# Optimization experiments

Hardware: AMD Instinct MI355X
Metric: run time of the kernel (lower is better)

## Reference

```python
import jax, jax.numpy as jnp
import numpy as np

RADIUS = 9.0   # search_raduis_scale * particle_radius
K = 20         # N_neighbor
HIDDEN = [512, 512, 512, 512]


def embed(x, n_freqs):
    freqs = 2.0 ** jnp.arange(n_freqs, dtype=x.dtype)      # [F]
    xf = x[..., None, :] * freqs[:, None]                  # [..., F, C]
    sc = jnp.stack([jnp.sin(xf), jnp.cos(xf)], axis=-2)    # [..., F, 2, C]
    return jnp.concatenate([x, sc.reshape(*x.shape[:-1], -1)], axis=-1)


def ball_query(q, p, radius, k):
    # pytorch3d semantics: first k points (by index order) with squared dist < radius^2;
    # padding slots get dists=0, idx=-1, nn=0.
    n = p.shape[0]
    d2 = jnp.sum((q[:, None, :] - p[None, :, :]) ** 2, axis=-1)   # [P,N]
    valid = d2 < radius * radius
    score = jnp.where(valid, -jnp.arange(n, dtype=q.dtype), -jnp.inf)
    top, idx = jax.lax.top_k(score, k)                            # first k valid indices
    found = top > -jnp.inf
    safe = jnp.clip(idx, 0, n - 1)
    dists = jnp.where(found, jnp.take_along_axis(d2, safe, axis=1), 0.0)
    nn = jnp.where(found[..., None], p[safe], 0.0)                # [P,K,3]
    return dists, jnp.where(found, idx, -1), nn


def mlp(x, params):
    n = len(params)
    for l, (v, g, b) in enumerate(params):
        w = g * v / jnp.linalg.norm(v, axis=1, keepdims=True)     # weight_norm, dim=0
        x = x @ w.T + b
        if l < n - 1:
            x = jax.nn.relu(x)
    return jax.nn.sigmoid(x)


def setup_inputs() -> dict:
    key = jax.random.key(0)
    ks = jax.random.split(key, 32)
    R, S, N, F = 256, 128, 4096, 256
    P = R * S
    inp = {
        "points": jax.random.normal(ks[0], (P, 3), dtype=jnp.float32) * 3.0,
        "normals": jax.random.normal(ks[1], (P, 3), dtype=jnp.float32),
        "view_dirs": jax.random.normal(ks[2], (P, 3), dtype=jnp.float32),
        "feature_vectors": jax.random.normal(ks[3], (P, F), dtype=jnp.float32),
        "phys_points": jax.random.normal(ks[4], (N, 3), dtype=jnp.float32) * 3.0,
        "ray_dirs": jax.random.normal(ks[5], (R, 3), dtype=jnp.float32),
        "cam_loc": jax.random.normal(ks[6], (1, 3), dtype=jnp.float32),
    }
    d0 = 3 + 3 + 3 + F + 63 + 9 + 63 + 63 + 27 + 27   # = 517
    dims = [d0] + HIDDEN + [3]
    for l in range(len(dims) - 1):
        fan_in, fan_out = dims[l], dims[l + 1]
        inp[f"v{l}"] = jax.random.normal(ks[7 + l], (fan_out, fan_in), dtype=jnp.float32) * float(np.sqrt(2.0 / fan_out))
        inp[f"g{l}"] = jnp.ones((fan_out, 1), dtype=jnp.float32)
        inp[f"b{l}"] = jnp.zeros((fan_out,), dtype=jnp.float32)
    return inp


def reference(points, normals, view_dirs, feature_vectors, phys_points, ray_dirs, cam_loc,
              v0, g0, b0, v1, g1, b1, v2, g2, b2, v3, g3, b3, v4, g4, b4):
    params = [(v0, g0, b0), (v1, g1, b1), (v2, g2, b2), (v3, g3, b3), (v4, g4, b4)]
    # mode == 'idr'
    rendering_input = jnp.concatenate([points, view_dirs, normals, feature_vectors], axis=-1)
    dists, idx, neighbors = ball_query(points, phys_points, RADIUS, K)
    nn_mask = dists != 0                                             # [P,K]
    num_nn = nn_mask.sum(-1, keepdims=True).astype(points.dtype)     # [P,1]
    # smoothing_position (exclude_ray=True): Euclidean dists recomputed incl. zero-padded slots
    dd = jnp.linalg.norm(neighbors - points[:, None, :], axis=-1)    # [P,K]
    w = jnp.maximum(1.0 - (dd / RADIUS) ** 3, 0.0)
    smoothed_pos = (w[..., None] * neighbors).sum(-2) / (w.sum(-1, keepdims=True) + 1e-12)
    density = w.sum(-1, keepdims=True)                               # [P,1]
    d = smoothed_pos - cam_loc                                       # broadcast [P,3]
    smoothed_dir = d / jnp.linalg.norm(d, axis=-1, keepdims=True)
    # variance of masked neighbor offsets
    vec = jnp.where(nn_mask[..., None], neighbors - points[:, None, :], 0.0)
    vec_mean = vec.sum(-2) / (num_nn + 1e-12)                        # [P,3]
    var = jnp.where(nn_mask[..., None], (vec - vec_mean[:, None, :]) ** 2, 0.0).sum(-2) / (num_nn + 1e-12)
    reps = points.shape[0] // ray_dirs.shape[0]                      # samples per ray
    hit_dir_emb = jnp.repeat(embed(ray_dirs, 4), reps, axis=0)       # [P,27]
    feats = jnp.concatenate([embed(points, 10), embed(density, 4), embed(smoothed_pos, 10),
                             embed(var, 10), hit_dir_emb, embed(smoothed_dir, 4)], axis=-1)
    x = jnp.concatenate([rendering_input, feats], axis=-1)           # [P,517]
    return mlp(x, params)
```

## Files before the change

kernel.cpp:

```cpp
#include <hip/hip_runtime.h>
#include <hip/hip_bf16.h>

typedef unsigned short u16;
typedef short short8 __attribute__((ext_vector_type(8)));
typedef unsigned short ushort8 __attribute__((ext_vector_type(8)));
typedef float f32x4 __attribute__((ext_vector_type(4)));

static __device__ __forceinline__ u16 f2bf(float f) {
  unsigned u = __builtin_bit_cast(unsigned, f);
  unsigned r = (u + 0x7fffu + ((u >> 16) & 1u)) >> 16;
  return (u16)r;
}
static __device__ __forceinline__ float bf2f(u16 h) {
  unsigned u = ((unsigned)h) << 16;
  return __builtin_bit_cast(float, u);
}

static __device__ __forceinline__ void gload_lds16(const u16* g, u16* l) {
  __builtin_amdgcn_global_load_lds(
      (const __attribute__((address_space(1))) void*)g,
      (__attribute__((address_space(3))) void*)l, 16, 0, 0);
}


static __device__ void prep_w0_body(const float* __restrict__ v,
                                    const float* __restrict__ g,
                                    u16* __restrict__ out, int row, int lane) {
  double s = 0.0;
  for (int k = lane; k < 517; k += 64) {
    double x = (double)v[(size_t)row * 517 + k];
    s += x * x;
  }
#pragma unroll
  for (int off = 32; off; off >>= 1) s += __shfl_xor(s, off);
  double scale = (double)g[row] / sqrt(s);

  for (int j = lane; j < 576; j += 64) {
    int orig = -1;
    if (j < 256) {
      orig = 9 + j;
    } else if (j < 281) {
      int e = j - 256;
      if (e < 9)       orig = e;
      else if (e < 12) orig = 265 + (e - 9);
      else if (e == 12) orig = 328;
      else if (e < 16) orig = 337 + (e - 13);
      else if (e < 19) orig = 400 + (e - 16);
      else if (e < 22) orig = 463 + (e - 19);
      else if (e < 25) orig = 490 + (e - 22);
    } else if (j >= 288 && j < 524) {
      int t = j - 288;
      if (t < 60)       orig = 268 + t;
      else if (t < 68)  orig = 329 + (t - 60);
      else if (t < 128) orig = 340 + (t - 68);
      else if (t < 188) orig = 403 + (t - 128);
      else if (t < 212) orig = 466 + (t - 188);
      else if (t < 236) orig = 493 + (t - 212);
    }
    float wv = (orig >= 0) ? (float)((double)v[(size_t)row * 517 + orig] * scale) : 0.0f;
    out[(size_t)row * 576 + j] = f2bf(wv);
  }
}

static __device__ void prep_w_body(const float* __restrict__ v,
                                   const float* __restrict__ g,
                                   u16* __restrict__ out, int row, int lane) {
  double s = 0.0;
  for (int k = lane; k < 512; k += 64) {
    double x = (double)v[(size_t)row * 512 + k];
    s += x * x;
  }
#pragma unroll
  for (int off = 32; off; off >>= 1) s += __shfl_xor(s, off);
  double scale = (double)g[row] / sqrt(s);
  for (int k = lane; k < 512; k += 64)
    out[(size_t)row * 512 + k] = f2bf((float)((double)v[(size_t)row * 512 + k] * scale));
}

static __device__ void prep_w4_body(const float* __restrict__ v,
                                    const float* __restrict__ g,
                                    float* __restrict__ out, int row, int lane) {
  double s = 0.0;
  for (int k = lane; k < 512; k += 64) {
    double x = (double)v[(size_t)row * 512 + k];
    s += x * x;
  }
#pragma unroll
  for (int off = 32; off; off >>= 1) s += __shfl_xor(s, off);
  double scale = (double)g[row] / sqrt(s);
  for (int k = lane; k < 512; k += 64)
    out[(size_t)row * 512 + k] = (float)((double)v[(size_t)row * 512 + k] * scale);
}

static __device__ void build_tb_body(u16* __restrict__ TB, int lane) {
  for (int i = lane; i < 320; i += 64) {
    const int j = 256 + i;
    unsigned d = 0;
    if (j < 281) {
      int e = j - 256;
      int src = -1;
      if (e < 9)       src = e;
      else if (e < 12) src = e - 9;
      else if (e == 12) src = 9;
      else if (e < 16) src = 10 + (e - 13);
      else if (e < 19) src = 13 + (e - 16);
      else if (e < 22) src = 16 + (e - 19);
      else if (e < 25) src = 19 + (e - 22);
      if (src >= 0) d = 1u | ((unsigned)src << 2);
    } else if (j >= 288 && j < 524) {
      int t = j - 288;
      if (t < 236) {
        int base, src0;
        if (t < 60)       { base = 0;   src0 = 0;  }
        else if (t < 68)  { base = 60;  src0 = 9;  }
        else if (t < 128) { base = 68;  src0 = 10; }
        else if (t < 188) { base = 128; src0 = 13; }
        else if (t < 212) { base = 188; src0 = 16; }
        else              { base = 212; src0 = 19; }
        int u = t - base;
        int f, cs, src;
        if (src0 == 9) { f = u >> 1; cs = u & 1; src = 9; }
        else { f = u / 6; int r = u - 6 * f; cs = (r >= 3) ? 1 : 0; src = src0 + (cs ? r - 3 : r); }
        d = 2u | ((unsigned)src << 2) | ((unsigned)cs << 7) | ((unsigned)f << 8);
      }
    }
    TB[i] = (u16)d;
  }
}

__global__ void prep_all(const float* __restrict__ v0, const float* __restrict__ g0,
                         const float* __restrict__ v1, const float* __restrict__ g1,
                         const float* __restrict__ v2, const float* __restrict__ g2,
                         const float* __restrict__ v3, const float* __restrict__ g3,
                         const float* __restrict__ v4, const float* __restrict__ g4,
                         u16* __restrict__ W0, u16* __restrict__ W1,
                         u16* __restrict__ W2, u16* __restrict__ W3,
                         float* __restrict__ W4, u16* __restrict__ TB) {
  const int b = blockIdx.x;
  const int lane = threadIdx.x;
  if (b < 512)       prep_w0_body(v0, g0, W0, b, lane);
  else if (b < 1024) prep_w_body(v1, g1, W1, b - 512, lane);
  else if (b < 1536) prep_w_body(v2, g2, W2, b - 1024, lane);
  else if (b < 2048) prep_w_body(v3, g3, W3, b - 1536, lane);
  else if (b == 2048) {
    for (int r = 0; r < 3; ++r) prep_w4_body(v4, g4, W4, r, lane);
  } else {
    build_tb_body(TB, lane);
  }
}

__global__ __launch_bounds__(256) void scan_kernel(
    const float* __restrict__ pts, const float* __restrict__ phys,
    u16* __restrict__ idxbuf) {
  const int m = (int)((blockIdx.x * blockDim.x + threadIdx.x) >> 6);
  const int lane = (int)(threadIdx.x & 63);

  const double qx = (double)pts[m * 3 + 0];
  const double qy = (double)pts[m * 3 + 1];
  const double qz = (double)pts[m * 3 + 2];

  u16* __restrict__ row = idxbuf + (size_t)m * 24;

  int found = 0;
  for (int base = 0; base < 4096 && found < 20; base += 64) {
    const int j = base + lane;
    const double px = (double)phys[j * 3 + 0];
    const double py = (double)phys[j * 3 + 1];
    const double pz = (double)phys[j * 3 + 2];
    const double dx = px - qx, dy = py - qy, dz = pz - qz;
    const double d2 = dx * dx + dy * dy + dz * dz;
    const bool valid = d2 < 81.0;
    const unsigned long long mb = __ballot(valid);
    const int rank = found + __popcll(mb & ((1ull << lane) - 1ull));
    if (valid && rank < 20) row[rank] = (u16)j;
    found += __popcll(mb);
    if (found > 20) found = 20;
  }
  if (lane == 0) row[20] = (u16)found;
}

__global__ __launch_bounds__(256) void gstats_kernel(
    const float* __restrict__ pts, const float* __restrict__ phys,
    const float* __restrict__ cam, const u16* __restrict__ idxbuf,
    float* __restrict__ Pbuf) {
  const int i = blockIdx.x * 256 + threadIdx.x;

  const double qx = (double)pts[i * 3 + 0];
  const double qy = (double)pts[i * 3 + 1];
  const double qz = (double)pts[i * 3 + 2];

  const u16* __restrict__ row = idxbuf + (size_t)i * 24;
  const int cnt = (int)row[20];

  int nnn = 0;
  double w_sum = 0, wpx = 0, wpy = 0, wpz = 0;
  double Sx = 0, Sy = 0, Sz = 0, Qx = 0, Qy = 0, Qz = 0;

#pragma unroll
  for (int s = 0; s < 20; ++s) {
    if (s < cnt) {
      const int j = (int)row[s];
      const double px = (double)phys[j * 3 + 0];
      const double py = (double)phys[j * 3 + 1];
      const double pz = (double)phys[j * 3 + 2];
      const double dx = px - qx, dy = py - qy, dz = pz - qz;
      const double d2 = dx * dx + dy * dy + dz * dz;
      const float d2f = (float)d2;
      float wf = 1.0f - d2f * sqrtf(d2f) * (1.0f / 729.0f);
      if (wf < 0.0f) wf = 0.0f;
      const double w = (double)wf;
      w_sum += w; wpx += w * px; wpy += w * py; wpz += w * pz;
      if (d2 != 0.0) {
        nnn += 1;
        Sx += dx; Sy += dy; Sz += dz;
        Qx += dx * dx; Qy += dy * dy; Qz += dz * dz;
      }
    }
  }

  {
    const float q2f = (float)(qx * qx + qy * qy + qz * qz);
    float wpad = 1.0f - q2f * sqrtf(q2f) * (1.0f / 729.0f);
    if (wpad < 0.0f) wpad = 0.0f;
    w_sum += (double)(20 - cnt) * (double)wpad;
  }

  const double inv_denom = 1.0 / (w_sum + 1e-12);
  const double sposx = wpx * inv_denom, sposy = wpy * inv_denom, sposz = wpz * inv_denom;

  const double inv_nd = 1.0 / ((double)nnn + 1e-12);
  const double vmx = Sx * inv_nd, vmy = Sy * inv_nd, vmz = Sz * inv_nd;
  const float vax = (float)((Qx - 2.0 * vmx * Sx + (double)nnn * vmx * vmx) * inv_nd);
  const float vay = (float)((Qy - 2.0 * vmy * Sy + (double)nnn * vmy * vmy) * inv_nd);
  const float vaz = (float)((Qz - 2.0 * vmz * Sz + (double)nnn * vmz * vmz) * inv_nd);

  const double ddx = sposx - (double)cam[0];
  const double ddy = sposy - (double)cam[1];
  const double ddz = sposz - (double)cam[2];
  const double inv_dnm = 1.0 / sqrt(ddx * ddx + ddy * ddy + ddz * ddz);

  f32x4* out = (f32x4*)(Pbuf + (size_t)i * 12);
  f32x4 o0, o1, o2;
  o0[0] = (float)w_sum; o0[1] = (float)sposx; o0[2] = (float)sposy; o0[3] = (float)sposz;
  o1[0] = vax; o1[1] = vay; o1[2] = vaz; o1[3] = (float)(ddx * inv_dnm);
  o2[0] = (float)(ddy * inv_dnm); o2[1] = (float)(ddz * inv_dnm); o2[2] = 0.0f; o2[3] = 0.0f;
  out[0] = o0; out[1] = o1; out[2] = o2;
}

__global__ __launch_bounds__(576) void emb_kernel(
    const float* __restrict__ pts, const float* __restrict__ nrm,
    const float* __restrict__ vdir, const float* __restrict__ fv,
    const float* __restrict__ rdir, const float* __restrict__ Pbuf,
    const u16* __restrict__ TB, u16* __restrict__ X) {
  const int cc = (int)threadIdx.x;
  const int y = (int)threadIdx.y;
  const int m = blockIdx.x * 8 + y;

  __shared__ float sc[8][24];
  if (cc < 22) {
    float v;
    if (cc < 3)       v = pts[m * 3 + cc];
    else if (cc < 6)  v = vdir[m * 3 + (cc - 3)];
    else if (cc < 9)  v = nrm[m * 3 + (cc - 6)];
    else if (cc < 10) v = Pbuf[(size_t)m * 12 + 0];
    else if (cc < 13) v = Pbuf[(size_t)m * 12 + 1 + (cc - 10)];
    else if (cc < 16) v = Pbuf[(size_t)m * 12 + 4 + (cc - 13)];
    else if (cc < 19) v = rdir[(m >> 7) * 3 + (cc - 16)];
    else              v = Pbuf[(size_t)m * 12 + 7 + (cc - 19)];
    sc[y][cc] = v;
  }
  __syncthreads();

  u16* __restrict__ xp = X + (size_t)m * 576 + cc * 8;

  if (cc < 32) {
    const f32x4* fp = (const f32x4*)(fv + (size_t)m * 256 + cc * 8);
    f32x4 a = fp[0], b = fp[1];
    short8 o;
    o[0] = (short)f2bf(a[0]); o[1] = (short)f2bf(a[1]);
    o[2] = (short)f2bf(a[2]); o[3] = (short)f2bf(a[3]);
    o[4] = (short)f2bf(b[0]); o[5] = (short)f2bf(b[1]);
    o[6] = (short)f2bf(b[2]); o[7] = (short)f2bf(b[3]);
    *(short8*)xp = o;
  } else {
    ushort8 tb = *(const ushort8*)(TB + (size_t)(cc - 32) * 8);
    short8 o;
#pragma unroll
    for (int e = 0; e < 8; ++e) {
      const unsigned d = (unsigned)tb[e];
      const unsigned kind = d & 3u;
      float val = 0.0f;
      if (kind) {
        float x = sc[y][(d >> 2) & 31u];
        if (kind == 2u) {
          x *= __builtin_bit_cast(float, (127u + (d >> 8)) << 23);
          float r = x * 0.15915494309189535f + (((d >> 7) & 1u) ? 0.25f : 0.0f);
          r -= floorf(r);
          val = __builtin_amdgcn_sinf(r);
        } else {
          val = x;
        }
      }
      o[e] = (short)f2bf(val);
    }
    *(short8*)xp = o;
  }
}

template <int KTILES, bool HEAD>
__global__ __launch_bounds__(512, 2) void gemm_relu(const u16* __restrict__ A,
                                                    const u16* __restrict__ B,
                                                    const float* __restrict__ bias,
                                                    u16* __restrict__ C,
                                                    const float* __restrict__ W4h,
                                                    float* __restrict__ Pp) {
  constexpr int K = KTILES * 64;
  constexpr int EPS = 264;
  __shared__ __align__(16) u16 smem[67584];
#define AS_(b, r) (smem + (size_t)(b) * 32768 + (size_t)(r) * 64)
#define BS_(b, r) (smem + (size_t)(b) * 32768 + 16384 + (size_t)(r) * 64)

  const int t = threadIdx.x;
  const int lane = t & 63;
  const int wid = t >> 6;
  const int wm = wid >> 2;
  const int wn = wid & 3;

  const int bid = blockIdx.x;
  const int wgid = (bid & 7) * 32 + (bid >> 3);
  const int n0 = (wgid & 1) * 256;
  const int m0 = (wgid >> 1) * 256;

  const int srow = lane >> 3;
  const int gcol = ((lane & 7) ^ srow) * 8;

  f32x4 acc[8][4] = {};

#define STAGE(kt, b)                                                           \
  {                                                                            \
    const int k0_ = (kt) * 64;                                                 \
    _Pragma("unroll")                                                          \
    for (int i_ = 0; i_ < 4; ++i_) {                                           \
      const int rbase_ = wid * 8 + i_ * 64;                                    \
      const int row_ = rbase_ + srow;                                          \
      gload_lds16(A + (size_t)(m0 + row_) * K + k0_ + gcol, AS_(b, rbase_));   \
      gload_lds16(B + (size_t)(n0 + row_) * K + k0_ + gcol, BS_(b, rbase_));   \
    }                                                                          \
  }

  STAGE(0, 0);

  const int rsw = lane & 7;
  for (int kt = 0; kt < KTILES; ++kt) {
    const int cur = kt & 1;
    __builtin_amdgcn_s_barrier();
    if (kt + 1 < KTILES) {
      STAGE(kt + 1, cur ^ 1);
      asm volatile("s_waitcnt vmcnt(8)" ::: "memory");
    } else {
      asm volatile("s_waitcnt vmcnt(0)" ::: "memory");
    }
    __builtin_amdgcn_s_barrier();
#pragma unroll
    for (int ks = 0; ks < 2; ++ks) {
      short8 af[8], bfv[4];
      const int fr = lane & 15;
      const int cc = ((ks * 4 + (lane >> 4)) ^ rsw) * 8;
#pragma unroll
      for (int f = 0; f < 8; ++f)
        af[f] = *(const short8*)(AS_(cur, wm * 128 + f * 16 + fr) + cc);
#pragma unroll
      for (int f = 0; f < 4; ++f)
        bfv[f] = *(const short8*)(BS_(cur, wn * 64 + f * 16 + fr) + cc);
#pragma unroll
      for (int fm = 0; fm < 8; ++fm)
#pragma unroll
        for (int fn = 0; fn < 4; ++fn)
          acc[fm][fn] = __builtin_amdgcn_mfma_f32_16x16x32_bf16(af[fm], bfv[fn], acc[fm][fn], 0, 0, 0);
    }
  }
#undef STAGE

  __syncthreads();
  const int lr = lane >> 4, lc = lane & 15;
#pragma unroll
  for (int fn = 0; fn < 4; ++fn) {
    const int tcol = wn * 64 + fn * 16 + lc;
    const float bv = bias[n0 + tcol];
#pragma unroll
    for (int fm = 0; fm < 8; ++fm) {
      const int rowb = wm * 128 + fm * 16 + lr * 4;
#pragma unroll
      for (int rg = 0; rg < 4; ++rg) {
        float vv = fmaxf(acc[fm][fn][rg] + bv, 0.0f);
        smem[(size_t)(rowb + rg) * EPS + tcol] = f2bf(vv);
      }
    }
  }
  __syncthreads();

  if (!HEAD) {
#pragma unroll
    for (int it = 0; it < 16; ++it) {
      const int row = wid * 32 + it * 2 + (lane >> 5);
      const int ch = lane & 31;
      short8 v = *(const short8*)(smem + (size_t)row * EPS + ch * 8);
      *(short8*)(C + (size_t)(m0 + row) * 512 + n0 + ch * 8) = v;
    }
  } else {
    const int row = t >> 1;
    const int half = t & 1;
    float s0 = 0.0f, s1 = 0.0f, s2 = 0.0f;
    const int cbase = half * 128;
#pragma unroll
    for (int ch = 0; ch < 16; ++ch) {
      short8 v = *(const short8*)(smem + (size_t)row * EPS + cbase + ch * 8);
#pragma unroll
      for (int e = 0; e < 8; ++e) {
        const float h = bf2f((u16)v[e]);
        const int col = n0 + cbase + ch * 8 + e;
        s0 += h * W4h[0 * 512 + col];
        s1 += h * W4h[1 * 512 + col];
        s2 += h * W4h[2 * 512 + col];
      }
    }
    s0 += __shfl_xor(s0, 1);
    s1 += __shfl_xor(s1, 1);
    s2 += __shfl_xor(s2, 1);
    if (half == 0) {
      float* p = Pp + ((size_t)(n0 >> 8) * 32768 + (m0 + row)) * 4;
      p[0] = s0; p[1] = s1; p[2] = s2;
    }
  }
#undef AS_
#undef BS_
}

__global__ __launch_bounds__(256) void sigmoid_kernel(const float* __restrict__ Pp,
                                                      const float* __restrict__ b4,
                                                      float* __restrict__ out) {
  const int m = blockIdx.x * 256 + threadIdx.x;
  const f32x4 p0 = *(const f32x4*)(Pp + (size_t)m * 4);
  const f32x4 p1 = *(const f32x4*)(Pp + (size_t)(32768 + m) * 4);
#pragma unroll
  for (int r = 0; r < 3; ++r) {
    const float v = p0[r] + p1[r] + b4[r];
    out[(size_t)m * 3 + r] = 1.0f / (1.0f + expf(-v));
  }
}

extern "C" void kernel_launch(void* const* d_in, const int* in_sizes, int n_in,
                              void* d_out, int out_size, void* d_ws, size_t ws_size,
                              hipStream_t stream) {
  const float* pts  = (const float*)d_in[0];
  const float* nrm  = (const float*)d_in[1];
  const float* vdir = (const float*)d_in[2];
  const float* fv   = (const float*)d_in[3];
  const float* phys = (const float*)d_in[4];
  const float* rdir = (const float*)d_in[5];
  const float* cam  = (const float*)d_in[6];
  const float* v0 = (const float*)d_in[7];  const float* g0 = (const float*)d_in[8];  const float* b0 = (const float*)d_in[9];
  const float* v1 = (const float*)d_in[10]; const float* g1 = (const float*)d_in[11]; const float* b1 = (const float*)d_in[12];
  const float* v2 = (const float*)d_in[13]; const float* g2 = (const float*)d_in[14]; const float* b2 = (const float*)d_in[15];
  const float* v3 = (const float*)d_in[16]; const float* g3 = (const float*)d_in[17]; const float* b3 = (const float*)d_in[18];
  const float* v4 = (const float*)d_in[19]; const float* g4 = (const float*)d_in[20]; const float* b4 = (const float*)d_in[21];

  char* ws = (char*)d_ws;
  u16*      W0 = (u16*)(ws + 0);
  u16*      W1 = (u16*)(ws + 589824);
  u16*      W2 = (u16*)(ws + 1114112);
  u16*      W3 = (u16*)(ws + 1638400);
  float*    W4 = (float*)(ws + 2162688);
  u16*      TB = (u16*)(ws + 2168832);
  u16*      Ix = (u16*)(ws + 2171136);
  float*    Pp = (float*)(ws + 2171136);
  float*    Pb = (float*)(ws + 3744000);
  u16*      X  = (u16*)(ws + 5316864);
  u16*      H1 = (u16*)(ws + 43065600);
  u16*      H2 = X;

  prep_all<<<2050, 64, 0, stream>>>(v0, g0, v1, g1, v2, g2, v3, g3, v4, g4,
                                    W0, W1, W2, W3, W4, TB);

  scan_kernel<<<8192, 256, 0, stream>>>(pts, phys, Ix);
  gstats_kernel<<<128, 256, 0, stream>>>(pts, phys, cam, Ix, Pb);
  emb_kernel<<<4096, dim3(72, 8), 0, stream>>>(pts, nrm, vdir, fv, rdir, Pb, TB, X);

  gemm_relu<9, false><<<256, 512, 0, stream>>>(X,  W0, b0, H1, nullptr, nullptr);
  gemm_relu<8, false><<<256, 512, 0, stream>>>(H1, W1, b1, H2, nullptr, nullptr);
  gemm_relu<8, false><<<256, 512, 0, stream>>>(H2, W2, b2, H1, nullptr, nullptr);
  gemm_relu<8, true ><<<256, 512, 0, stream>>>(H1, W3, b3, nullptr, W4, Pp);

  sigmoid_kernel<<<128, 256, 0, stream>>>(Pp, b4, (float*)d_out);
}
```

Measured before the change: 153.4 us.

## Restructure GEMM mainloop into 4-slot K-half ring buffer with single barrier

Splits each 64-wide K tile into two 32-wide halves staged through a 4-slot LDS ring, prefetching two halves ahead so each iteration needs only one barrier instead of two. It also changes the LDS swizzle to match 32-element rows, streams A fragments one at a time to reduce register pressure, and raises wave priority around the MFMA block. The aim is better overlap of global-to-LDS loads with MFMA work and fewer stalls at barriers. In exchange there are more loop iterations with fewer MFMAs each, and a single barrier per slot relies on the slot count to avoid overwriting data that is still being read.

```diff
diff --git a/kernel.cpp b/kernel.cpp
--- a/kernel.cpp
+++ b/kernel.cpp
@@ -315,10 +315,9 @@
                                                     const float* __restrict__ W4h,
                                                     float* __restrict__ Pp) {
   constexpr int K = KTILES * 64;
+  constexpr int NKH = KTILES * 2;
   constexpr int EPS = 264;
   __shared__ __align__(16) u16 smem[67584];
-#define AS_(b, r) (smem + (size_t)(b) * 32768 + (size_t)(r) * 64)
-#define BS_(b, r) (smem + (size_t)(b) * 32768 + 16384 + (size_t)(r) * 64)
 
   const int t = threadIdx.x;
   const int lane = t & 63;
@@ -331,55 +330,60 @@
   const int n0 = (wgid & 1) * 256;
   const int m0 = (wgid >> 1) * 256;
 
-  const int srow = lane >> 3;
-  const int gcol = ((lane & 7) ^ srow) * 8;
+  const int gk = ((lane & 3) ^ ((lane >> 3) & 3)) * 8;
+  const int srow = lane >> 2;
 
   f32x4 acc[8][4] = {};
 
-#define STAGE(kt, b)                                                           \
+#define STAGE_KH(j_)                                                           \
   {                                                                            \
-    const int k0_ = (kt) * 64;                                                 \
+    const int sl_ = (j_) & 3;                                                  \
+    const int k0_ = (j_) * 32;                                                 \
     _Pragma("unroll")                                                          \
-    for (int i_ = 0; i_ < 4; ++i_) {                                           \
-      const int rbase_ = wid * 8 + i_ * 64;                                    \
-      const int row_ = rbase_ + srow;                                          \
-      gload_lds16(A + (size_t)(m0 + row_) * K + k0_ + gcol, AS_(b, rbase_));   \
-      gload_lds16(B + (size_t)(n0 + row_) * K + k0_ + gcol, BS_(b, rbase_));   \
+    for (int l_ = 0; l_ < 2; ++l_) {                                           \
+      const int row_ = l_ * 128 + wid * 16 + srow;                             \
+      u16* db_ = smem + sl_ * 8192 + (l_ * 512 + wid * 64) * 8;                \
+      gload_lds16(A + (size_t)(m0 + row_) * K + k0_ + gk, db_);                \
+      gload_lds16(B + (size_t)(n0 + row_) * K + k0_ + gk, db_ + 32768);       \
     }                                                                          \
   }
 
-  STAGE(0, 0);
-
-  const int rsw = lane & 7;
-  for (int kt = 0; kt < KTILES; ++kt) {
-    const int cur = kt & 1;
-    __builtin_amdgcn_s_barrier();
-    if (kt + 1 < KTILES) {
-      STAGE(kt + 1, cur ^ 1);
+  STAGE_KH(0);
+  STAGE_KH(1);
+
+  const int fr = lane & 15;
+  const int hi = lane >> 4;
+  const int rsw2 = (fr >> 1) & 3;
+  const int cofs = (hi ^ rsw2) * 8;
+
+  for (int j = 0; j < NKH; ++j) {
+    if (j + 2 < NKH) {
+      STAGE_KH(j + 2);
       asm volatile("s_waitcnt vmcnt(8)" ::: "memory");
+    } else if (j + 1 < NKH) {
+      asm volatile("s_waitcnt vmcnt(4)" ::: "memory");
     } else {
       asm volatile("s_waitcnt vmcnt(0)" ::: "memory");
     }
     __builtin_amdgcn_s_barrier();
-#pragma unroll
-    for (int ks = 0; ks < 2; ++ks) {
-      short8 af[8], bfv[4];
-      const int fr = lane & 15;
-      const int cc = ((ks * 4 + (lane >> 4)) ^ rsw) * 8;
-#pragma unroll
-      for (int f = 0; f < 8; ++f)
-        af[f] = *(const short8*)(AS_(cur, wm * 128 + f * 16 + fr) + cc);
-#pragma unroll
-      for (int f = 0; f < 4; ++f)
-        bfv[f] = *(const short8*)(BS_(cur, wn * 64 + f * 16 + fr) + cc);
-#pragma unroll
-      for (int fm = 0; fm < 8; ++fm)
-#pragma unroll
-        for (int fn = 0; fn < 4; ++fn)
-          acc[fm][fn] = __builtin_amdgcn_mfma_f32_16x16x32_bf16(af[fm], bfv[fn], acc[fm][fn], 0, 0, 0);
-    }
-  }
-#undef STAGE
+
+    const int abase = (j & 3) * 8192;
+    const int bbase = 32768 + abase;
+    short8 bfv[4];
+#pragma unroll
+    for (int fn = 0; fn < 4; ++fn)
+      bfv[fn] = *(const short8*)(smem + bbase + (wn * 64 + fn * 16 + fr) * 32 + cofs);
+    __builtin_amdgcn_s_setprio(1);
+#pragma unroll
+    for (int fm = 0; fm < 8; ++fm) {
+      short8 af = *(const short8*)(smem + abase + (wm * 128 + fm * 16 + fr) * 32 + cofs);
+#pragma unroll
+      for (int fn = 0; fn < 4; ++fn)
+        acc[fm][fn] = __builtin_amdgcn_mfma_f32_16x16x32_bf16(af, bfv[fn], acc[fm][fn], 0, 0, 0);
+    }
+    __builtin_amdgcn_s_setprio(0);
+  }
+#undef STAGE_KH
 
   __syncthreads();
   const int lr = lane >> 4, lc = lane & 15;
@@ -432,8 +436,6 @@
       p[0] = s0; p[1] = s1; p[2] = s2;
     }
   }
-#undef AS_
-#undef BS_
 }
 
 __global__ __launch_bounds__(256) void sigmoid_kernel(const float* __restrict__ Pp,
```

After: 155.9 us. About the same (+1.6%).

## Fuse ball-query scan and neighbor statistics into one wave-per-query kernel

Applied to the files above, without the earlier changes.

Merges the neighbor scan and the statistics kernel. Each lane now accumulates weighted sums and variance terms for the valid neighbors it finds, and a wave-wide shuffle reduction combines them, so the index buffer and its write/read round trip go away. The old gstats stage ran one thread per query over only 128 blocks, so its serial double-precision loop was poorly parallelised. The cost is ten double-precision shuffle reductions per wave, a different floating-point summation order, and work done only by lane 0 for the final outputs.

```diff
diff --git a/kernel.cpp b/kernel.cpp
--- a/kernel.cpp
+++ b/kernel.cpp
@@ -149,9 +149,9 @@
   }
 }
 
-__global__ __launch_bounds__(256) void scan_kernel(
+__global__ __launch_bounds__(256) void sg_kernel(
     const float* __restrict__ pts, const float* __restrict__ phys,
-    u16* __restrict__ idxbuf) {
+    const float* __restrict__ cam, float* __restrict__ Pbuf) {
   const int m = (int)((blockIdx.x * blockDim.x + threadIdx.x) >> 6);
   const int lane = (int)(threadIdx.x & 63);
 
@@ -159,9 +159,10 @@
   const double qy = (double)pts[m * 3 + 1];
   const double qz = (double)pts[m * 3 + 2];
 
-  u16* __restrict__ row = idxbuf + (size_t)m * 24;
-
-  int found = 0;
+  int found = 0, nnn = 0;
+  double w_sum = 0, wpx = 0, wpy = 0, wpz = 0;
+  double Sx = 0, Sy = 0, Sz = 0, Qx = 0, Qy = 0, Qz = 0;
+
   for (int base = 0; base < 4096 && found < 20; base += 64) {
     const int j = base + lane;
     const double px = (double)phys[j * 3 + 0];
@@ -172,39 +173,7 @@
     const bool valid = d2 < 81.0;
     const unsigned long long mb = __ballot(valid);
     const int rank = found + __popcll(mb & ((1ull << lane) - 1ull));
-    if (valid && rank < 20) row[rank] = (u16)j;
-    found += __popcll(mb);
-    if (found > 20) found = 20;
-  }
-  if (lane == 0) row[20] = (u16)found;
-}
-
-__global__ __launch_bounds__(256) void gstats_kernel(
-    const float* __restrict__ pts, const float* __restrict__ phys,
-    const float* __restrict__ cam, const u16* __restrict__ idxbuf,
-    float* __restrict__ Pbuf) {
-  const int i = blockIdx.x * 256 + threadIdx.x;
-
-  const double qx = (double)pts[i * 3 + 0];
-  const double qy = (double)pts[i * 3 + 1];
-  const double qz = (double)pts[i * 3 + 2];
-
-  const u16* __restrict__ row = idxbuf + (size_t)i * 24;
-  const int cnt = (int)row[20];
-
-  int nnn = 0;
-  double w_sum = 0, wpx = 0, wpy = 0, wpz = 0;
-  double Sx = 0, Sy = 0, Sz = 0, Qx = 0, Qy = 0, Qz = 0;
-
-#pragma unroll
-  for (int s = 0; s < 20; ++s) {
-    if (s < cnt) {
-      const int j = (int)row[s];
-      const double px = (double)phys[j * 3 + 0];
-      const double py = (double)phys[j * 3 + 1];
-      const double pz = (double)phys[j * 3 + 2];
-      const double dx = px - qx, dy = py - qy, dz = pz - qz;
-      const double d2 = dx * dx + dy * dy + dz * dz;
+    if (valid && rank < 20) {
       const float d2f = (float)d2;
       float wf = 1.0f - d2f * sqrtf(d2f) * (1.0f / 729.0f);
       if (wf < 0.0f) wf = 0.0f;
@@ -216,13 +185,24 @@
         Qx += dx * dx; Qy += dy * dy; Qz += dz * dz;
       }
     }
+    found += __popcll(mb);
+    if (found > 20) found = 20;
+  }
+
+#pragma unroll
+  for (int off = 32; off; off >>= 1) {
+    w_sum += __shfl_xor(w_sum, off);
+    wpx += __shfl_xor(wpx, off); wpy += __shfl_xor(wpy, off); wpz += __shfl_xor(wpz, off);
+    Sx += __shfl_xor(Sx, off); Sy += __shfl_xor(Sy, off); Sz += __shfl_xor(Sz, off);
+    Qx += __shfl_xor(Qx, off); Qy += __shfl_xor(Qy, off); Qz += __shfl_xor(Qz, off);
+    nnn += __shfl_xor(nnn, off);
   }
 
   {
     const float q2f = (float)(qx * qx + qy * qy + qz * qz);
     float wpad = 1.0f - q2f * sqrtf(q2f) * (1.0f / 729.0f);
     if (wpad < 0.0f) wpad = 0.0f;
-    w_sum += (double)(20 - cnt) * (double)wpad;
+    w_sum += (double)(20 - found) * (double)wpad;
   }
 
   const double inv_denom = 1.0 / (w_sum + 1e-12);
@@ -239,12 +219,14 @@
   const double ddz = sposz - (double)cam[2];
   const double inv_dnm = 1.0 / sqrt(ddx * ddx + ddy * ddy + ddz * ddz);
 
-  f32x4* out = (f32x4*)(Pbuf + (size_t)i * 12);
-  f32x4 o0, o1, o2;
-  o0[0] = (float)w_sum; o0[1] = (float)sposx; o0[2] = (float)sposy; o0[3] = (float)sposz;
-  o1[0] = vax; o1[1] = vay; o1[2] = vaz; o1[3] = (float)(ddx * inv_dnm);
-  o2[0] = (float)(ddy * inv_dnm); o2[1] = (float)(ddz * inv_dnm); o2[2] = 0.0f; o2[3] = 0.0f;
-  out[0] = o0; out[1] = o1; out[2] = o2;
+  if (lane == 0) {
+    f32x4* out = (f32x4*)(Pbuf + (size_t)m * 12);
+    f32x4 o0, o1, o2;
+    o0[0] = (float)w_sum; o0[1] = (float)sposx; o0[2] = (float)sposy; o0[3] = (float)sposz;
+    o1[0] = vax; o1[1] = vay; o1[2] = vaz; o1[3] = (float)(ddx * inv_dnm);
+    o2[0] = (float)(ddy * inv_dnm); o2[1] = (float)(ddz * inv_dnm); o2[2] = 0.0f; o2[3] = 0.0f;
+    out[0] = o0; out[1] = o1; out[2] = o2;
+  }
 }
 
 __global__ __launch_bounds__(576) void emb_kernel(
@@ -472,7 +454,6 @@
   u16*      W3 = (u16*)(ws + 1638400);
   float*    W4 = (float*)(ws + 2162688);
   u16*      TB = (u16*)(ws + 2168832);
-  u16*      Ix = (u16*)(ws + 2171136);
   float*    Pp = (float*)(ws + 2171136);
   float*    Pb = (float*)(ws + 3744000);
   u16*      X  = (u16*)(ws + 5316864);
@@ -482,8 +463,7 @@
   prep_all<<<2050, 64, 0, stream>>>(v0, g0, v1, g1, v2, g2, v3, g3, v4, g4,
                                     W0, W1, W2, W3, W4, TB);
 
-  scan_kernel<<<8192, 256, 0, stream>>>(pts, phys, Ix);
-  gstats_kernel<<<128, 256, 0, stream>>>(pts, phys, cam, Ix, Pb);
+  sg_kernel<<<8192, 256, 0, stream>>>(pts, phys, cam, Pb);
   emb_kernel<<<4096, dim3(72, 8), 0, stream>>>(pts, nrm, vdir, fv, rdir, Pb, TB, X);
 
   gemm_relu<9, false><<<256, 512, 0, stream>>>(X,  W0, b0, H1, nullptr, nullptr);
```

After: 177.1 us. 1.15x slower.
